# Kernel tuning notes

Measured on AMD Instinct MI355X. Metric: run time of the kernel, lower is better.

The kernel has to match this reference:

```python
import jax, jax.numpy as jnp
import numpy as np

# Static graph dimensions (mirror mat_wann config)
B, IN_DIM, NH, NO = 16384, 512, 128, 256
DENSITY = 0.03


def _build_adjacency():
    """Build the static sparse connectivity matrix.

    mat is [NH + NO, IN_DIM + NH]; entry values: 0 = no edge, 1 = linear edge
    (weight only), 2/3/4 = weight then tanh/relu/sigmoid. Hidden rows only read
    input columns (hidden->hidden block zero), output rows read inputs+hiddens.
    Edge order (for weight assignment) is row-major, as in the torch module.
    """
    rng = np.random.default_rng(0)
    p = DENSITY
    probs = [1.0 - p, p / 4, p / 4, p / 4, p / 4]
    mat_h = rng.choice(5, size=(NH, IN_DIM), p=probs)            # hidden rows (input cols only)
    mat_o = rng.choice(5, size=(NO, IN_DIM + NH), p=probs)       # output rows
    rows_h, cols_h = np.nonzero(mat_h)
    acts_h = mat_h[rows_h, cols_h]
    rows_o, cols_o = np.nonzero(mat_o)
    acts_o = mat_o[rows_o, cols_o]
    return (rows_h.astype(np.int32), cols_h.astype(np.int32), acts_h.astype(np.int32),
            rows_o.astype(np.int32), cols_o.astype(np.int32), acts_o.astype(np.int32))


def setup_inputs() -> dict:
    rows_h, cols_h, acts_h, rows_o, cols_o, acts_o = _build_adjacency()
    key = jax.random.key(0)
    kx, kh, ko = jax.random.split(key, 3)
    x = jax.random.normal(kx, (B, IN_DIM), dtype=jnp.float32)
    # one learned scalar weight per edge (nn.Linear(1,1,bias=False) each)
    wh = jax.random.normal(kh, (rows_h.shape[0],), dtype=jnp.float32) * 0.5
    wo = jax.random.normal(ko, (rows_o.shape[0],), dtype=jnp.float32) * 0.5
    return {
        "x": x, "wh": wh, "wo": wo,
        "rows_h": jnp.asarray(rows_h), "cols_h": jnp.asarray(cols_h), "acts_h": jnp.asarray(acts_h),
        "rows_o": jnp.asarray(rows_o), "cols_o": jnp.asarray(cols_o), "acts_o": jnp.asarray(acts_o),
    }


def _edge_act(z, acts):
    # act id 1 -> identity (weight only); 2 -> tanh; 3 -> relu; 4 -> sigmoid
    return jnp.where(acts == 2, jnp.tanh(z),
           jnp.where(acts == 3, jax.nn.relu(z),
           jnp.where(acts == 4, jax.nn.sigmoid(z), z)))


def reference(x, wh, wo, rows_h, cols_h, acts_h, rows_o, cols_o, acts_o):
    # hidden nodes: per-edge scalar weight + per-edge activation, scatter-add to dest
    zh = _edge_act(x[:, cols_h] * wh, acts_h)                     # [B, Eh]
    H = jnp.zeros((x.shape[0], NH), x.dtype).at[:, rows_h].add(zh)  # [B, NH]
    src = jnp.concatenate([x, H], axis=1)                         # [B, IN+NH]
    zo = _edge_act(src[:, cols_o] * wo, acts_o)                   # [B, Eo]
    out = jnp.zeros((x.shape[0], NO), x.dtype).at[:, rows_o].add(zo)
    return jnp.tanh(out)                                          # output_activation
```

## Files before the change

### kernel.cpp

```cpp
#include <hip/hip_runtime.h>
#include <math.h>

#define BATCH   16384
#define IN_DIM  512
#define NH      128
#define NO      256
#define L2E     1.4426950408889634f

__device__ __forceinline__ float fast_rcp(float x) { return __builtin_amdgcn_rcpf(x); }
__device__ __forceinline__ float fast_exp2(float x) {
#if __has_builtin(__builtin_amdgcn_exp2f)
    return __builtin_amdgcn_exp2f(x);
#else
    return exp2f(x);
#endif
}
__device__ __forceinline__ int rfl(int v) { return __builtin_amdgcn_readfirstlane(v); }
__device__ __forceinline__ int rdl(int v, int l) { return __builtin_amdgcn_readlane(v, l); }

__device__ __forceinline__ float fast_tanh(float z) {
    float ex = fast_exp2(2.f * L2E * z);
    return 1.f - 2.f * fast_rcp(1.f + ex);
}
__device__ __forceinline__ float act_k(int a) {
    return (a == 2) ? (2.f * L2E) : ((a == 4) ? -L2E : 0.f);
}

__device__ __forceinline__ unsigned int f2bf_rne(float f) {
    unsigned int u = __float_as_uint(f);
    return (u + 0x7FFFu + ((u >> 16) & 1u)) >> 16;
}
__device__ __forceinline__ float bf2f(unsigned short h) { return __uint_as_float(((unsigned int)h) << 16); }
__device__ __forceinline__ unsigned short f2bf16s(float f) { return (unsigned short)f2bf_rne(f); }

__device__ __forceinline__ int lower_bound_dev(const int* __restrict__ arr, int n, int v) {
    int lo = 0, hi = n;
    while (lo < hi) { int m = (lo + hi) >> 1; if (arr[m] < v) lo = m + 1; else hi = m; }
    return lo;
}

#define FXS     514
#define FHS     65
#define MLDS    99072
#define RSTRIDE 128

__global__ __launch_bounds__(512)
void prep_rows(const int* __restrict__ rows_h, const int* __restrict__ cols_h,
               const int* __restrict__ acts_h, const float* __restrict__ wh,
               const int* __restrict__ rows_o, const int* __restrict__ cols_o,
               const int* __restrict__ acts_o, const float* __restrict__ wo,
               int Eh, int Eo, uint2* __restrict__ rrh, uint2* __restrict__ rro)
{
    const int lane = (int)(threadIdx.x & 63);
    const int wid  = (int)((blockIdx.x * 512 + threadIdx.x) >> 6);
    if (wid >= NH + NO) return;
    const bool isH = wid < NH;
    const int r = isH ? wid : wid - NH;
    const int*   rows = isH ? rows_h : rows_o;
    const int*   cols = isH ? cols_h : cols_o;
    const int*   acts = isH ? acts_h : acts_o;
    const float* ww   = isH ? wh : wo;
    const int    E    = isH ? Eh : Eo;
    uint2* rec = (isH ? rrh : rro) + (size_t)r * RSTRIDE;

    const int e0 = lower_bound_dev(rows, E, r);
    const int e1 = lower_bound_dev(rows, E, r + 1);
    int n = e1 - e0; if (n > 127) n = 127;
    const unsigned long long lt = (1ull << lane) - 1ull;

    int cnt[8] = {0,0,0,0,0,0,0,0};
    for (int g = 0; g < n; g += 64) {
        int seg = -1;
        if (g + lane < n) {
            int e = e0 + g + lane;
            int a = acts[e];
            int col = cols[e];
            seg = (a - 1) + ((!isH && col >= IN_DIM) ? 4 : 0);
        }
        #pragma unroll
        for (int s = 0; s < 8; ++s) cnt[s] += __popcll(__ballot(seg == s));
    }
    int cum[9]; cum[0] = 0;
    #pragma unroll
    for (int s = 0; s < 8; ++s) cum[s + 1] = cum[s] + cnt[s];
    if (lane == 0) {
        unsigned hx = (unsigned)cum[1] | ((unsigned)cum[2] << 8) | ((unsigned)cum[3] << 16) | ((unsigned)cum[4] << 24);
        unsigned hy = (unsigned)cum[5] | ((unsigned)cum[6] << 8) | ((unsigned)cum[7] << 16) | ((unsigned)n << 24);
        rec[0] = make_uint2(hx, hy);
    }
    int pos[8];
    #pragma unroll
    for (int s = 0; s < 8; ++s) pos[s] = cum[s];
    for (int g = 0; g < n; g += 64) {
        int seg = -1; unsigned offv = 0, wbits = 0;
        if (g + lane < n) {
            int e = e0 + g + lane;
            int a = acts[e];
            int col = cols[e];
            bool hs = (!isH && col >= IN_DIM);
            seg = (a - 1) + (hs ? 4 : 0);
            offv = hs ? (unsigned)((col - IN_DIM) * FHS) : (unsigned)col;
            float w = ww[e];
            float ws = (a == 2) ? (2.f * L2E) * w : ((a == 4) ? -L2E * w : w);
            wbits = __float_as_uint(ws);
        }
        #pragma unroll
        for (int s = 0; s < 8; ++s) {
            unsigned long long m = __ballot(seg == s);
            if (seg == s) {
                int slot = 1 + pos[s] + __popcll(m & lt);
                rec[slot] = make_uint2(offv, wbits);
            }
            pos[s] += __popcll(m);
        }
    }
}

template<int ACT, bool HSRC>
__device__ __forceinline__ void seg_run(float& acc, const unsigned short* __restrict__ X,
                                        const float* __restrict__ Hf,
                                        uint2 hv, int lo, int hi, int lane)
{
    #pragma unroll 2
    for (int j = lo; j < hi; ++j) {
        int soff = rdl((int)hv.x, j + 1);
        float w  = __uint_as_float((unsigned)rdl((int)hv.y, j + 1));
        float v;
        if (HSRC) v = Hf[soff + lane];
        else      v = bf2f(X[lane * FXS + soff]);
        if (ACT == 1)      acc = fmaf(v, w, acc);
        else if (ACT == 2) { float ex = fast_exp2(v * w); acc += 1.f - 2.f * fast_rcp(1.f + ex); }
        else if (ACT == 3) acc += fmaxf(v * w, 0.f);
        else               { float ex = fast_exp2(v * w); acc += fast_rcp(1.f + ex); }
    }
}

template<bool OUT>
__device__ __forceinline__ float row_body(uint2 hv, const uint2* __restrict__ grow,
                                          const unsigned short* __restrict__ X,
                                          const float* __restrict__ Hf, int lane)
{
    const int ux = rdl((int)hv.x, 0), uy = rdl((int)hv.y, 0);
    const int c1 = ux & 255, c2 = (ux >> 8) & 255, c3 = (ux >> 16) & 255, c4 = (int)((unsigned)ux >> 24);
    const int c5 = uy & 255, c6 = (uy >> 8) & 255, c7 = (uy >> 16) & 255, n  = (int)((unsigned)uy >> 24);
    float acc = 0.f;
    if (n <= 63) {
        seg_run<1,false>(acc, X, Hf, hv, 0,  c1, lane);
        seg_run<2,false>(acc, X, Hf, hv, c1, c2, lane);
        seg_run<3,false>(acc, X, Hf, hv, c2, c3, lane);
        seg_run<4,false>(acc, X, Hf, hv, c3, c4, lane);
        if (OUT) {
            seg_run<1,true>(acc, X, Hf, hv, c4, c5, lane);
            seg_run<2,true>(acc, X, Hf, hv, c5, c6, lane);
            seg_run<3,true>(acc, X, Hf, hv, c6, c7, lane);
            seg_run<4,true>(acc, X, Hf, hv, c7, n,  lane);
        }
    } else {
        for (int j = 0; j < n; ++j) {
            int soff = rfl((int)grow[1 + j].x);
            float w  = __int_as_float(rfl((int)grow[1 + j].y));
            int seg = (j < c1) ? 0 : (j < c2) ? 1 : (j < c3) ? 2 : (j < c4) ? 3
                    : (j < c5) ? 4 : (j < c6) ? 5 : (j < c7) ? 6 : 7;
            float v = (seg >= 4) ? Hf[soff + lane] : bf2f(X[lane * FXS + soff]);
            int a = (seg & 3) + 1;
            if (a == 1) acc = fmaf(v, w, acc);
            else if (a == 2) { float ex = fast_exp2(v * w); acc += 1.f - 2.f * fast_rcp(1.f + ex); }
            else if (a == 3) acc += fmaxf(v * w, 0.f);
            else { float ex = fast_exp2(v * w); acc += fast_rcp(1.f + ex); }
        }
    }
    return acc;
}

__global__ __launch_bounds__(1024)
void fused_main(const float* __restrict__ x,
                const uint2* __restrict__ rrh, const uint2* __restrict__ rro,
                float* __restrict__ out)
{
    extern __shared__ char lds[];
    unsigned short* X  = (unsigned short*)lds;
    float*          Hf = (float*)(lds + 65792);
    const int tid  = (int)threadIdx.x;
    const int lane = tid & 63;
    const int wv   = tid >> 6;
    const int rb   = (int)blockIdx.x * 64;

    {
        const float4* xv = (const float4*)(x + (size_t)rb * IN_DIM);
        #pragma unroll
        for (int kk = 0; kk < 8; ++kk) {
            int v = tid + kk * 1024;
            int rr = v >> 7, i = v & 127;
            float4 f = xv[v];
            unsigned int lo = f2bf_rne(f.x) | (f2bf_rne(f.y) << 16);
            unsigned int hi = f2bf_rne(f.z) | (f2bf_rne(f.w) << 16);
            unsigned int* dst = (unsigned int*)&X[rr * FXS + i * 4];
            dst[0] = lo; dst[1] = hi;
        }
    }
    __syncthreads();

    {
        uint2 hv = rrh[(size_t)(wv * 8) * RSTRIDE + lane];
        for (int q = 0; q < 8; ++q) {
            const int r = wv * 8 + q;
            uint2 hvn = hv;
            if (q < 7) hvn = rrh[(size_t)(r + 1) * RSTRIDE + lane];
            float acc = row_body<false>(hv, rrh + (size_t)r * RSTRIDE, X, Hf, lane);
            Hf[r * FHS + lane] = acc;
            hv = hvn;
        }
    }
    __syncthreads();

    {
        uint2 hv = rro[(size_t)(wv * 16) * RSTRIDE + lane];
        #pragma unroll 1
        for (int qc = 0; qc < 4; ++qc) {
            float r4[4];
            #pragma unroll
            for (int qi = 0; qi < 4; ++qi) {
                const int q = qc * 4 + qi;
                const int r = wv * 16 + q;
                uint2 hvn = hv;
                if (q < 15) hvn = rro[(size_t)(r + 1) * RSTRIDE + lane];
                r4[qi] = fast_tanh(row_body<true>(hv, rro + (size_t)r * RSTRIDE, X, Hf, lane));
                hv = hvn;
            }
            *(float4*)&out[(size_t)(rb + lane) * NO + wv * 16 + qc * 4] =
                make_float4(r4[0], r4[1], r4[2], r4[3]);
        }
    }
}

#define FT      1024
#define FBPB    64
#define FHS2    65
#define FOBTS   260
#define FLDS    (99072 + 1544)
__device__ __forceinline__ float edge_act2(float z, int a, float k) {
    float ex = fast_exp2(k * z);
    float rc = fast_rcp(1.f + ex);
    return (a == 2) ? (1.f - 2.f * rc) : ((a == 4) ? rc : ((a == 3) ? fmaxf(z, 0.f) : z));
}
__global__ __launch_bounds__(FT)
void wann_fused(const float* __restrict__ x,
                const int* __restrict__ rows_h, const int* __restrict__ cols_h,
                const int* __restrict__ acts_h, const float* __restrict__ wh,
                const int* __restrict__ rows_o, const int* __restrict__ cols_o,
                const int* __restrict__ acts_o, const float* __restrict__ wo,
                float* __restrict__ out, int Eh, int Eo)
{
    extern __shared__ char lds[];
    unsigned short* X   = (unsigned short*)lds;
    float*          H   = (float*)(lds + 65792);
    float*          OBT = (float*)lds;
    int*            offsH = (int*)(lds + 99072);
    int*            offsO = offsH + (NH + 1);
    const int tid  = threadIdx.x;
    const int lane = tid & 63;
    const int wv   = tid >> 6;
    const int rb   = blockIdx.x * FBPB;
    const int* wh_i = (const int*)wh;
    const int* wo_i = (const int*)wo;
    {
        const float4* xv = (const float4*)(x + (size_t)rb * IN_DIM);
        #pragma unroll
        for (int kk = 0; kk < (FBPB * IN_DIM / 4) / FT; ++kk) {
            int v = tid + kk * FT;
            int r = v >> 7, i = v & 127;
            float4 f = xv[v];
            unsigned int lo = (unsigned int)f2bf16s(f.x) | ((unsigned int)f2bf16s(f.y) << 16);
            unsigned int hi = (unsigned int)f2bf16s(f.z) | ((unsigned int)f2bf16s(f.w) << 16);
            unsigned int* dst = (unsigned int*)&X[r * FXS + i * 4];
            dst[0] = lo; dst[1] = hi;
        }
    }
    if (tid <= NH) offsH[tid] = lower_bound_dev(rows_h, Eh, tid);
    else if (tid <= NH + 1 + NO) offsO[tid - (NH + 1)] = lower_bound_dev(rows_o, Eo, tid - (NH + 1));
    __syncthreads();
    for (int r = wv * (NH / 16); r < (wv + 1) * (NH / 16); ++r) {
        const int e0 = rfl(offsH[r]); const int e1 = rfl(offsH[r + 1]);
        float acc = 0.f;
        #pragma unroll 4
        for (int e = e0; e < e1; ++e) {
            int col = rfl(cols_h[e]); int a = rfl(acts_h[e]);
            float w = __int_as_float(rfl(wh_i[e]));
            acc += edge_act2(bf2f(X[lane * FXS + col]) * w, a, act_k(a));
        }
        H[r * FHS2 + lane] = acc;
    }
    __syncthreads();
    float res[NO / 16];
    #pragma unroll
    for (int rr = 0; rr < NO / 16; ++rr) {
        const int r = wv * (NO / 16) + rr;
        const int e0 = rfl(offsO[r]); const int e1 = rfl(offsO[r + 1]);
        float acc = 0.f;
        #pragma unroll 4
        for (int e = e0; e < e1; ++e) {
            int col = rfl(cols_o[e]); int a = rfl(acts_o[e]);
            float w = __int_as_float(rfl(wo_i[e]));
            float v = (col < IN_DIM) ? bf2f(X[lane * FXS + col]) : H[(col - IN_DIM) * FHS2 + lane];
            acc += edge_act2(v * w, a, act_k(a));
        }
        res[rr] = fast_tanh(acc);
    }
    __syncthreads();
    #pragma unroll
    for (int rr = 0; rr < NO / 16; ++rr)
        OBT[lane * FOBTS + wv * (NO / 16) + rr] = res[rr];
    __syncthreads();
    #pragma unroll
    for (int kk = 0; kk < (FBPB * NO / 4) / FT; ++kk) {
        int v = tid + kk * FT;
        int c4 = v & 63, b = v >> 6;
        float4 o = *(const float4*)&OBT[b * FOBTS + c4 * 4];
        *(float4*)&out[(size_t)(rb + b) * NO + c4 * 4] = o;
    }
}

extern "C" void kernel_launch(void* const* d_in, const int* in_sizes, int n_in,
                              void* d_out, int out_size, void* d_ws, size_t ws_size,
                              hipStream_t stream) {
    const float* x      = (const float*)d_in[0];
    const float* wh     = (const float*)d_in[1];
    const float* wo     = (const float*)d_in[2];
    const int*   rows_h = (const int*)d_in[3];
    const int*   cols_h = (const int*)d_in[4];
    const int*   acts_h = (const int*)d_in[5];
    const int*   rows_o = (const int*)d_in[6];
    const int*   cols_o = (const int*)d_in[7];
    const int*   acts_o = (const int*)d_in[8];
    float*       out    = (float*)d_out;

    const int Eh = in_sizes[1];
    const int Eo = in_sizes[2];

    char*  ws  = (char*)d_ws;
    uint2* rrh = (uint2*)ws;
    uint2* rro = (uint2*)(ws + (size_t)NH * RSTRIDE * 8);
    size_t need = (size_t)(NH + NO) * RSTRIDE * 8;

    if (ws_size >= need) {
        prep_rows<<<(NH + NO) * 64 / 512, 512, 0, stream>>>(
            rows_h, cols_h, acts_h, wh, rows_o, cols_o, acts_o, wo,
            Eh, Eo, rrh, rro);
        fused_main<<<BATCH / 64, 1024, MLDS, stream>>>(x, rrh, rro, out);
    } else {
        wann_fused<<<BATCH / FBPB, FT, FLDS, stream>>>(
            x, rows_h, cols_h, acts_h, wh, rows_o, cols_o, acts_o, wo, out, Eh, Eo);
    }
}
```

Before: 144.1 us.

## Stage output tile through LDS for coalesced stores and unroll edge gathers

Output results are now kept per thread, then transposed through shared memory (reusing the X region) so each wave writes contiguous output rows, instead of each lane issuing a strided float4 store. The per-segment edge loop is unrolled by four so the gathers are issued before the activation math, which adds instruction-level parallelism. Per-lane base pointers into X and H are hoisted out of the loop. The trade-offs are an extra barrier and LDS round trip. The res array is indexed inside a loop marked unroll 1, so it may be placed in scratch memory.

Result: slower. 147.0 us (+2.0%).

```diff
diff --git a/kernel.cpp b/kernel.cpp
--- a/kernel.cpp
+++ b/kernel.cpp
@@ -116,44 +116,67 @@
     }
 }
 
+template<int ACT>
+__device__ __forceinline__ float edge_apply(float acc, float v, float w) {
+    if (ACT == 1)      return fmaf(v, w, acc);
+    else if (ACT == 2) { float ex = fast_exp2(v * w); return acc + (1.f - 2.f * fast_rcp(1.f + ex)); }
+    else if (ACT == 3) return acc + fmaxf(v * w, 0.f);
+    else               { float ex = fast_exp2(v * w); return acc + fast_rcp(1.f + ex); }
+}
+
 template<int ACT, bool HSRC>
-__device__ __forceinline__ void seg_run(float& acc, const unsigned short* __restrict__ X,
-                                        const float* __restrict__ Hf,
-                                        uint2 hv, int lo, int hi, int lane)
-{
+__device__ __forceinline__ void seg_run(float& acc,
+                                        const unsigned short* __restrict__ Xl,
+                                        const float* __restrict__ Hl,
+                                        uint2 hv, int lo, int hi)
+{
+    int j = lo;
     #pragma unroll 2
-    for (int j = lo; j < hi; ++j) {
-        int soff = rdl((int)hv.x, j + 1);
-        float w  = __uint_as_float((unsigned)rdl((int)hv.y, j + 1));
-        float v;
-        if (HSRC) v = Hf[soff + lane];
-        else      v = bf2f(X[lane * FXS + soff]);
-        if (ACT == 1)      acc = fmaf(v, w, acc);
-        else if (ACT == 2) { float ex = fast_exp2(v * w); acc += 1.f - 2.f * fast_rcp(1.f + ex); }
-        else if (ACT == 3) acc += fmaxf(v * w, 0.f);
-        else               { float ex = fast_exp2(v * w); acc += fast_rcp(1.f + ex); }
+    for (; j + 3 < hi; j += 4) {
+        int o0 = rdl((int)hv.x, j + 1);
+        int o1 = rdl((int)hv.x, j + 2);
+        int o2 = rdl((int)hv.x, j + 3);
+        int o3 = rdl((int)hv.x, j + 4);
+        float v0 = HSRC ? Hl[o0] : bf2f(Xl[o0]);
+        float v1 = HSRC ? Hl[o1] : bf2f(Xl[o1]);
+        float v2 = HSRC ? Hl[o2] : bf2f(Xl[o2]);
+        float v3 = HSRC ? Hl[o3] : bf2f(Xl[o3]);
+        float w0 = __uint_as_float((unsigned)rdl((int)hv.y, j + 1));
+        float w1 = __uint_as_float((unsigned)rdl((int)hv.y, j + 2));
+        float w2 = __uint_as_float((unsigned)rdl((int)hv.y, j + 3));
+        float w3 = __uint_as_float((unsigned)rdl((int)hv.y, j + 4));
+        acc = edge_apply<ACT>(acc, v0, w0);
+        acc = edge_apply<ACT>(acc, v1, w1);
+        acc = edge_apply<ACT>(acc, v2, w2);
+        acc = edge_apply<ACT>(acc, v3, w3);
+    }
+    for (; j < hi; ++j) {
+        int o = rdl((int)hv.x, j + 1);
+        float v = HSRC ? Hl[o] : bf2f(Xl[o]);
+        float w = __uint_as_float((unsigned)rdl((int)hv.y, j + 1));
+        acc = edge_apply<ACT>(acc, v, w);
     }
 }
 
 template<bool OUT>
 __device__ __forceinline__ float row_body(uint2 hv, const uint2* __restrict__ grow,
-                                          const unsigned short* __restrict__ X,
-                                          const float* __restrict__ Hf, int lane)
+                                          const unsigned short* __restrict__ Xl,
+                                          const float* __restrict__ Hl)
 {
     const int ux = rdl((int)hv.x, 0), uy = rdl((int)hv.y, 0);
     const int c1 = ux & 255, c2 = (ux >> 8) & 255, c3 = (ux >> 16) & 255, c4 = (int)((unsigned)ux >> 24);
     const int c5 = uy & 255, c6 = (uy >> 8) & 255, c7 = (uy >> 16) & 255, n  = (int)((unsigned)uy >> 24);
     float acc = 0.f;
     if (n <= 63) {
-        seg_run<1,false>(acc, X, Hf, hv, 0,  c1, lane);
-        seg_run<2,false>(acc, X, Hf, hv, c1, c2, lane);
-        seg_run<3,false>(acc, X, Hf, hv, c2, c3, lane);
-        seg_run<4,false>(acc, X, Hf, hv, c3, c4, lane);
+        seg_run<1,false>(acc, Xl, Hl, hv, 0,  c1);
+        seg_run<2,false>(acc, Xl, Hl, hv, c1, c2);
+        seg_run<3,false>(acc, Xl, Hl, hv, c2, c3);
+        seg_run<4,false>(acc, Xl, Hl, hv, c3, c4);
         if (OUT) {
-            seg_run<1,true>(acc, X, Hf, hv, c4, c5, lane);
-            seg_run<2,true>(acc, X, Hf, hv, c5, c6, lane);
-            seg_run<3,true>(acc, X, Hf, hv, c6, c7, lane);
-            seg_run<4,true>(acc, X, Hf, hv, c7, n,  lane);
+            seg_run<1,true>(acc, Xl, Hl, hv, c4, c5);
+            seg_run<2,true>(acc, Xl, Hl, hv, c5, c6);
+            seg_run<3,true>(acc, Xl, Hl, hv, c6, c7);
+            seg_run<4,true>(acc, Xl, Hl, hv, c7, n);
         }
     } else {
         for (int j = 0; j < n; ++j) {
@@ -161,7 +184,7 @@
             float w  = __int_as_float(rfl((int)grow[1 + j].y));
             int seg = (j < c1) ? 0 : (j < c2) ? 1 : (j < c3) ? 2 : (j < c4) ? 3
                     : (j < c5) ? 4 : (j < c6) ? 5 : (j < c7) ? 6 : 7;
-            float v = (seg >= 4) ? Hf[soff + lane] : bf2f(X[lane * FXS + soff]);
+            float v = (seg >= 4) ? Hl[soff] : bf2f(Xl[soff]);
             int a = (seg & 3) + 1;
             if (a == 1) acc = fmaf(v, w, acc);
             else if (a == 2) { float ex = fast_exp2(v * w); acc += 1.f - 2.f * fast_rcp(1.f + ex); }
@@ -178,12 +201,15 @@
                 float* __restrict__ out)
 {
     extern __shared__ char lds[];
-    unsigned short* X  = (unsigned short*)lds;
-    float*          Hf = (float*)(lds + 65792);
+    unsigned short* X   = (unsigned short*)lds;
+    float*          Hf  = (float*)(lds + 65792);
+    float*          OBT = (float*)lds;
     const int tid  = (int)threadIdx.x;
     const int lane = tid & 63;
     const int wv   = tid >> 6;
     const int rb   = (int)blockIdx.x * 64;
+    const unsigned short* Xl = X + (size_t)lane * FXS;
+    const float*          Hl = Hf + lane;
 
     {
         const float4* xv = (const float4*)(x + (size_t)rb * IN_DIM);
@@ -206,29 +232,38 @@
             const int r = wv * 8 + q;
             uint2 hvn = hv;
             if (q < 7) hvn = rrh[(size_t)(r + 1) * RSTRIDE + lane];
-            float acc = row_body<false>(hv, rrh + (size_t)r * RSTRIDE, X, Hf, lane);
+            float acc = row_body<false>(hv, rrh + (size_t)r * RSTRIDE, Xl, Hl);
             Hf[r * FHS + lane] = acc;
             hv = hvn;
         }
     }
     __syncthreads();
 
+    float res[NO / 16];
     {
         uint2 hv = rro[(size_t)(wv * 16) * RSTRIDE + lane];
         #pragma unroll 1
-        for (int qc = 0; qc < 4; ++qc) {
-            float r4[4];
-            #pragma unroll
-            for (int qi = 0; qi < 4; ++qi) {
-                const int q = qc * 4 + qi;
-                const int r = wv * 16 + q;
-                uint2 hvn = hv;
-                if (q < 15) hvn = rro[(size_t)(r + 1) * RSTRIDE + lane];
-                r4[qi] = fast_tanh(row_body<true>(hv, rro + (size_t)r * RSTRIDE, X, Hf, lane));
-                hv = hvn;
-            }
-            *(float4*)&out[(size_t)(rb + lane) * NO + wv * 16 + qc * 4] =
-                make_float4(r4[0], r4[1], r4[2], r4[3]);
+        for (int q = 0; q < 16; ++q) {
+            const int r = wv * 16 + q;
+            uint2 hvn = hv;
+            if (q < 15) hvn = rro[(size_t)(r + 1) * RSTRIDE + lane];
+            res[q] = fast_tanh(row_body<true>(hv, rro + (size_t)r * RSTRIDE, Xl, Hl));
+            hv = hvn;
+        }
+    }
+    __syncthreads();
+
+    #pragma unroll
+    for (int q = 0; q < NO / 16; ++q)
+        OBT[(wv * (NO / 16) + q) * FHS + lane] = res[q];
+    __syncthreads();
+    #pragma unroll
+    for (int s = 0; s < 4; ++s) {
+        const int b = wv * 4 + s;
+        #pragma unroll
+        for (int i = 0; i < 4; ++i) {
+            const int c = lane + i * 64;
+            out[(size_t)(rb + b) * NO + c] = OBT[c * FHS + b];
         }
     }
 }
```
